# Performance work log

Hardware: AMD Instinct MI355X
Metric: run time of the kernel (lower is better)

The kernel has to match this reference:

```python
import jax, jax.numpy as jnp
import numpy as np

NOT_EPSILON = 1.0

def swishmax(x, axis):
    # x * exp(x - max) normalized by sum(|.|) + 1 over `axis`
    xexp = x * jnp.exp(x - jnp.max(x, axis=axis, keepdims=True))
    return xexp / (jnp.sum(jnp.abs(xexp), axis=axis, keepdims=True) + NOT_EPSILON)

def setup_inputs() -> dict:
    key = jax.random.key(0)
    ks = jax.random.split(key, 8)
    B, S, D = 2, 512, 256
    std = 0.02
    x = jax.random.normal(ks[0], (B, S, D), dtype=jnp.float32)
    w_pre = jax.random.normal(ks[1], (D, D), dtype=jnp.float32) * std
    w_q   = jax.random.normal(ks[2], (D, D), dtype=jnp.float32) * std
    w_k   = jax.random.normal(ks[3], (D, D), dtype=jnp.float32) * std
    w_va  = jax.random.normal(ks[4], (D, D), dtype=jnp.float32) * std
    w_al  = jax.random.normal(ks[5], (D, D), dtype=jnp.float32) * std
    w_vo  = jax.random.normal(ks[6], (D, D), dtype=jnp.float32) * std
    w_end = jax.random.normal(ks[7], (D, D), dtype=jnp.float32) * std
    return {"x": x, "w_pre": w_pre, "w_q": w_q, "w_k": w_k,
            "w_va": w_va, "w_al": w_al, "w_vo": w_vo, "w_end": w_end}

def reference(x, w_pre, w_q, w_k, w_va, w_al, w_vo, w_end):
    # pre: module_1d = Linear(D, D, bias=False)
    X = x @ w_pre.T                                    # [B,S,D]
    # FractalAttention depth=2 (base case): row_dims=(-3,)
    q = X + X @ w_q.T                                  # residual query proj
    k = X + X @ w_k.T                                  # residual key proj
    # batchify: key lhs -> [B,Sk,1,D], query rhs -> [B,1,Sq,D]
    raw = k[:, :, None, :] * q[:, None, :, :]          # [B,Sk,Sq,D]
    logits = raw + raw @ w_al.T                        # residual logit proj over D
    scale = swishmax(logits, axis=-3)                  # normalize over Sk
    v = X + X @ w_va.T
    vs = v[:, :, None, :] * scale                      # [B,Sk,Sq,D]
    vsum = jnp.sum(vs, axis=-3)                        # [B,Sq,D]
    vout = vsum + vsum @ w_vo.T
    X = X + vout                                       # transformer residual
    X = X @ w_end.T                                    # end: module_1d
    return X
```

## Files before the change

### kernel.cpp

```cpp
#include <hip/hip_runtime.h>
#include <hip/hip_bf16.h>


typedef __attribute__((ext_vector_type(8))) short short8;
typedef __attribute__((ext_vector_type(4))) float f32x4;
typedef __attribute__((ext_vector_type(8))) _Float16 half8;
typedef __attribute__((ext_vector_type(4))) _Float16 half4;

#define DD 256
#define SS 512
#define LOG2E 1.4426950408889634f
#define LN2   0.6931471805599453f

__device__ __forceinline__ unsigned short f2bf(float f) {
  unsigned int b = __float_as_uint(f);
  b += 0x7FFFu + ((b >> 16) & 1u);
  return (unsigned short)(b >> 16);
}
__device__ __forceinline__ short8 cvt8(f32x4 lo, f32x4 hi) {
  short8 r;
  r[0]=(short)f2bf(lo[0]); r[1]=(short)f2bf(lo[1]);
  r[2]=(short)f2bf(lo[2]); r[3]=(short)f2bf(lo[3]);
  r[4]=(short)f2bf(hi[0]); r[5]=(short)f2bf(hi[1]);
  r[6]=(short)f2bf(hi[2]); r[7]=(short)f2bf(hi[3]);
  return r;
}
__device__ __forceinline__ void gload16(const void* g, void* l) {
  __builtin_amdgcn_global_load_lds(
      (const __attribute__((address_space(1))) void*)g,
      (__attribute__((address_space(3))) void*)l,
      16, 0, 0);
}

__global__ __launch_bounds__(256) void prep_weights(
    const float* __restrict__ w0, const float* __restrict__ w1,
    const float* __restrict__ w2, const float* __restrict__ w3,
    const float* __restrict__ w4, const float* __restrict__ w5,
    const float* __restrict__ wal, unsigned short* __restrict__ out)
{
  const int bi = blockIdx.x;
  const int m = bi >> 5;
  const int off = ((bi & 31) * 256 + threadIdx.x) * 8;
  const float* src = m==0?w0: m==1?w1: m==2?w2: m==3?w3: m==4?w4: m==5?w5: wal;
  f32x4 a = *(const f32x4*)(src + off);
  f32x4 b = *(const f32x4*)(src + off + 4);
  if (m == 6) {
    const int e = off >> 8, d = off & 255;
#pragma unroll
    for (int jj = 0; jj < 4; ++jj) {
      if (e == d + jj)     a[jj] += 1.0f;
      if (e == d + 4 + jj) b[jj] += 1.0f;
    }
    half8 h;
#pragma unroll
    for (int jj = 0; jj < 4; ++jj) {
      h[jj]     = (_Float16)a[jj];
      h[jj + 4] = (_Float16)b[jj];
    }
    *(half8*)(out + (size_t)m * 65536 + off) = h;
  } else {
    *(short8*)(out + (size_t)m * 65536 + off) = cvt8(a, b);
  }
}

__global__ __launch_bounds__(256) void linear_bf(
    const float* __restrict__ A, const unsigned short* __restrict__ Wbf,
    const float* __restrict__ res1, const float* __restrict__ res2,
    float* __restrict__ out)
{
  const int bi = blockIdx.x;
  const int rb = (bi >> 2) * 16;
  const int cb = (bi & 3) * 64;
  const int tid = threadIdx.x;
  const int wv = tid >> 6, lane = tid & 63;
  const int g = lane >> 4, c = lane & 15;
  const int arow = rb + c;
  const int wrow = cb + wv * 16 + c;

  f32x4 acc = (f32x4){0.f, 0.f, 0.f, 0.f};
#pragma unroll
  for (int ks = 0; ks < 8; ++ks) {
    const int d0 = ks * 32 + g * 8;
    f32x4 a0 = *(const f32x4*)(A + arow * DD + d0);
    f32x4 a1 = *(const f32x4*)(A + arow * DD + d0 + 4);
    short8 av = cvt8(a0, a1);
    short8 bv = *(const short8*)(Wbf + wrow * DD + d0);
    acc = __builtin_amdgcn_mfma_f32_16x16x32_bf16(av, bv, acc, 0, 0, 0);
  }
#pragma unroll
  for (int j = 0; j < 4; ++j) {
    const int ro = rb + g * 4 + j;
    const int co = cb + wv * 16 + c;
    float v = acc[j];
    if (res1) v += res1[ro * DD + co];
    if (res2) v += res2[ro * DD + co];
    out[ro * DD + co] = v;
  }
}

__global__ __launch_bounds__(256) void linear_qkv(
    const float* __restrict__ X,
    const unsigned short* __restrict__ Wq, const unsigned short* __restrict__ Wk,
    const unsigned short* __restrict__ Wv,
    _Float16* __restrict__ qout, _Float16* __restrict__ kout,
    _Float16* __restrict__ vout)
{
  const int bi = blockIdx.x;
  const int rb = (bi >> 2) * 16;
  const int cb = (bi & 3) * 64;
  const int tid = threadIdx.x;
  const int wv = tid >> 6, lane = tid & 63;
  const int g = lane >> 4, c = lane & 15;
  const int arow = rb + c;
  const int wrow = cb + wv * 16 + c;

  f32x4 aq = (f32x4){0.f,0.f,0.f,0.f};
  f32x4 ak = (f32x4){0.f,0.f,0.f,0.f};
  f32x4 av_ = (f32x4){0.f,0.f,0.f,0.f};
#pragma unroll
  for (int ks = 0; ks < 8; ++ks) {
    const int d0 = ks * 32 + g * 8;
    f32x4 a0 = *(const f32x4*)(X + arow * DD + d0);
    f32x4 a1 = *(const f32x4*)(X + arow * DD + d0 + 4);
    short8 af = cvt8(a0, a1);
    short8 bq = *(const short8*)(Wq + wrow * DD + d0);
    aq = __builtin_amdgcn_mfma_f32_16x16x32_bf16(af, bq, aq, 0, 0, 0);
    short8 bk = *(const short8*)(Wk + wrow * DD + d0);
    ak = __builtin_amdgcn_mfma_f32_16x16x32_bf16(af, bk, ak, 0, 0, 0);
    short8 bv = *(const short8*)(Wv + wrow * DD + d0);
    av_ = __builtin_amdgcn_mfma_f32_16x16x32_bf16(af, bv, av_, 0, 0, 0);
  }
#pragma unroll
  for (int j = 0; j < 4; ++j) {
    const int ro = rb + g * 4 + j;
    const int co = cb + wv * 16 + c;
    const float base = X[ro * DD + co];
    qout[ro * DD + co] = (_Float16)((base + aq[j]) * LOG2E);
    kout[ro * DD + co] = (_Float16)(base + ak[j]);
    vout[ro * DD + co] = (_Float16)(base + av_[j]);
  }
}

__global__ __launch_bounds__(256) void pack_kv(
    const _Float16* __restrict__ k, const _Float16* __restrict__ v,
    _Float16* __restrict__ kfrag, _Float16* __restrict__ vfrag)
{
  const int id = blockIdx.x * 256 + threadIdx.x;
  if (id < 32768) {
    const int lane = id & 63, ks = (id >> 6) & 7, t2 = (id >> 9) & 31, b = id >> 14;
    const int g = lane >> 4, c = lane & 15;
    const _Float16* src = k + ((size_t)(b * SS + t2 * 16 + c) * DD + ks * 32 + g * 8);
    *(half8*)(kfrag + (size_t)id * 8) = *(const half8*)src;
  } else {
    const int id2 = id - 32768;
    const int lane = id2 & 63, i = (id2 >> 6) & 1, slice = (id2 >> 7) & 7,
              t2 = (id2 >> 10) & 31, b = id2 >> 15;
    const int g = lane >> 4, c = lane & 15;
    const _Float16* src = v + ((size_t)(b * SS + t2 * 16 + c) * DD + slice * 32 + i * 16 + g * 4);
    *(half4*)(vfrag + (size_t)id2 * 4) = *(const half4*)src;
  }
}

__global__ __launch_bounds__(256, 3) void fractal_attn(
    const _Float16* __restrict__ walI,
    const _Float16* __restrict__ qf,
    const _Float16* __restrict__ kfrag,
    const _Float16* __restrict__ vfrag,
    float* __restrict__ vsum)
{
  __shared__ _Float16 kt[2][4096];

  const int bid = blockIdx.x;
  const int eh = bid & 1;
  const int sq = (bid >> 1) & 511;
  const int b  = bid >> 10;
  const int tid = threadIdx.x;
  const int wv = tid >> 6;
  const int lane = tid & 63;
  const int g = lane >> 4, c = lane & 15;
  const int slice = eh * 4 + wv;
  const int sbase = slice * 32;

  const _Float16* ktile0 = kfrag + (size_t)b * 131072;
  auto stage = [&](int t) {
    const _Float16* src = ktile0 + (size_t)t * 4096;
    _Float16* dst = &kt[t & 1][0];
    gload16(src + tid * 8,        dst + tid * 8);
    gload16(src + 2048 + tid * 8, dst + 2048 + tid * 8);
  };

  stage(0);

  half8 afrag[2][8];
  {
    const _Float16* qrow = qf + (size_t)(b * SS + sq) * DD;
    half8 q8[8];
#pragma unroll
    for (int ks = 0; ks < 8; ++ks)
      q8[ks] = *(const half8*)(qrow + ks * 32 + g * 8);
#pragma unroll
    for (int i = 0; i < 2; ++i) {
      const int e = sbase + i * 16 + c;
      const _Float16* wrow = walI + (size_t)e * DD;
#pragma unroll
      for (int ks = 0; ks < 8; ++ks)
        afrag[i][ks] = (*(const half8*)(wrow + ks * 32 + g * 8)) * q8[ks];
    }
  }

  const _Float16* vfb = vfrag + (size_t)b * 131072 + slice * 512 + lane * 4;

  float mst[8], sst[8], vst[8];
#pragma unroll
  for (int s = 0; s < 8; ++s) { mst[s] = -1e30f; sst[s] = 0.f; vst[s] = 0.f; }

  half8 bf[8];
  half4 vqA[2], vqB[2];
  f32x4 accA[2], accB[2];
  const f32x4 zeroc = (f32x4){0.f, 0.f, 0.f, 0.f};

#define DSREAD(BUF)                                                 \
  {                                                                 \
    const _Float16* kb_ = &kt[BUF][0];                              \
    _Pragma("unroll")                                               \
    for (int ks = 0; ks < 8; ++ks)                                  \
      bf[ks] = *(const half8*)(kb_ + ks * 512 + lane * 8);          \
  }
#define LOADV(T2, VQ)                                               \
  {                                                                 \
    const _Float16* vf_ = vfb + (size_t)(T2) * 4096;                \
    VQ[0] = *(const half4*)(vf_);                                   \
    VQ[1] = *(const half4*)(vf_ + 256);                             \
  }
#define MFMA_INTO(ACC)                                              \
  {                                                                 \
    __builtin_amdgcn_s_setprio(1);                                  \
    ACC[0] = __builtin_amdgcn_mfma_f32_16x16x32_f16(                \
        afrag[0][0], bf[0], zeroc, 0, 0, 0);                        \
    ACC[1] = __builtin_amdgcn_mfma_f32_16x16x32_f16(                \
        afrag[1][0], bf[0], zeroc, 0, 0, 0);                        \
    _Pragma("unroll")                                               \
    for (int ks = 1; ks < 8; ++ks) {                                \
      ACC[0] = __builtin_amdgcn_mfma_f32_16x16x32_f16(              \
          afrag[0][ks], bf[ks], ACC[0], 0, 0, 0);                   \
      ACC[1] = __builtin_amdgcn_mfma_f32_16x16x32_f16(              \
          afrag[1][ks], bf[ks], ACC[1], 0, 0, 0);                   \
    }                                                               \
    __builtin_amdgcn_s_setprio(0);                                  \
  }
#define UPDATE(ACC, VQ)                                             \
  {                                                                 \
    _Pragma("unroll")                                               \
    for (int i = 0; i < 2; ++i)                                     \
      _Pragma("unroll")                                             \
      for (int j = 0; j < 4; ++j) {                                 \
        const int s = i * 4 + j;                                    \
        const float L = ACC[i][j];                                  \
        mst[s] = fmaxf(mst[s], L);                                  \
        const float p = L * __builtin_amdgcn_exp2f(L);              \
        sst[s] += fabsf(p);                                         \
        vst[s] = fmaf((float)VQ[i][j], p, vst[s]);                  \
      }                                                             \
  }

  LOADV(0, vqA);
  __syncthreads();
  DSREAD(0);
  stage(1);
  MFMA_INTO(accA);

#pragma unroll 1
  for (int t = 1; t < 31; t += 2) {
    __syncthreads();
    DSREAD(t & 1);
    LOADV(t, vqB);
    stage(t + 1);
    MFMA_INTO(accB);
    UPDATE(accA, vqA);

    __syncthreads();
    DSREAD((t + 1) & 1);
    LOADV(t + 1, vqA);
    if (t + 2 < 32) stage(t + 2);
    MFMA_INTO(accA);
    UPDATE(accB, vqB);
  }

  __syncthreads();
  DSREAD(1);
  LOADV(31, vqB);
  MFMA_INTO(accB);
  UPDATE(accA, vqA);
  UPDATE(accB, vqB);

#undef DSREAD
#undef LOADV
#undef MFMA_INTO
#undef UPDATE

#pragma unroll
  for (int mask = 1; mask <= 8; mask <<= 1) {
#pragma unroll
    for (int s = 0; s < 8; ++s) {
      mst[s] = fmaxf(mst[s], __shfl_xor(mst[s], mask));
      sst[s] += __shfl_xor(sst[s], mask);
      vst[s] += __shfl_xor(vst[s], mask);
    }
  }

  if (c == 0) {
    float* orow = vsum + (size_t)(b * SS + sq) * DD;
#pragma unroll
    for (int i = 0; i < 2; ++i) {
      f32x4 o;
#pragma unroll
      for (int j = 0; j < 4; ++j) {
        const int s = i * 4 + j;
        const float tt = LN2 * __builtin_amdgcn_exp2f(-mst[s]);
        o[j] = vst[s] * tt / (sst[s] * tt + 1.0f);
      }
      *(f32x4*)(orow + sbase + i * 16 + g * 4) = o;
    }
  }
}

extern "C" void kernel_launch(void* const* d_in, const int* in_sizes, int n_in,
                              void* d_out, int out_size, void* d_ws, size_t ws_size,
                              hipStream_t stream) {
  const float* x     = (const float*)d_in[0];
  const float* w_pre = (const float*)d_in[1];
  const float* w_q   = (const float*)d_in[2];
  const float* w_k   = (const float*)d_in[3];
  const float* w_va  = (const float*)d_in[4];
  const float* w_al  = (const float*)d_in[5];
  const float* w_vo  = (const float*)d_in[6];
  const float* w_end = (const float*)d_in[7];
  float* out = (float*)d_out;

  char* ws = (char*)d_ws;
  float*    X     = (float*)(ws);
  float*    Y     = (float*)(ws + (1 << 20));
  float*    vsum  = (float*)(ws + (2 << 20));
  _Float16* qf16  = (_Float16*)(ws + (3 << 20));
  _Float16* kf16  = (_Float16*)(ws + (3 << 20) + (512 << 10));
  _Float16* vf16  = (_Float16*)(ws + (4 << 20));
  _Float16* kfrag = (_Float16*)(ws + (4 << 20) + (512 << 10));
  _Float16* vfrag = (_Float16*)(ws + (5 << 20));
  unsigned short* wbf = (unsigned short*)(ws + (5 << 20) + (512 << 10));

  prep_weights<<<224, 256, 0, stream>>>(w_pre, w_q, w_k, w_va, w_vo, w_end,
                                        w_al, wbf);
  linear_bf<<<256, 256, 0, stream>>>(x, wbf + 0 * 65536, nullptr, nullptr, X);
  linear_qkv<<<256, 256, 0, stream>>>(X, wbf + 1 * 65536, wbf + 2 * 65536,
                                      wbf + 3 * 65536, qf16, kf16, vf16);
  pack_kv<<<384, 256, 0, stream>>>(kf16, vf16, kfrag, vfrag);
  fractal_attn<<<2048, 256, 0, stream>>>((const _Float16*)(wbf + 6 * 65536),
                                         qf16, kfrag, vfrag, vsum);
  linear_bf<<<256, 256, 0, stream>>>(vsum, wbf + 4 * 65536, vsum, X, Y);
  linear_bf<<<256, 256, 0, stream>>>(Y, wbf + 5 * 65536, nullptr, nullptr, out);
}
```

Before: 120.5 us.

## Stage V tiles through LDS with a four-deep async prefetch pipeline

Deepens the K-tile LDS ring from two to four buffers and adds a matching LDS ring for V fragments. V was previously read directly from global memory per wave; it is now loaded asynchronously alongside K, three tiles ahead. Plain __syncthreads is replaced by explicit vmcnt waits plus s_barrier so loads can stay in flight across iterations. This aims to hide global-memory latency behind the MFMA and exp work. In exchange it uses more LDS per block, which may limit occupancy, and the hand-counted waitcnt values must stay consistent with the number of loads issued.

```diff
diff --git a/kernel.cpp b/kernel.cpp
--- a/kernel.cpp
+++ b/kernel.cpp
@@ -168,7 +168,8 @@
     const _Float16* __restrict__ vfrag,
     float* __restrict__ vsum)
 {
-  __shared__ _Float16 kt[2][4096];
+  __shared__ _Float16 kt[4][4096];
+  __shared__ _Float16 vt[4][2048];
 
   const int bid = blockIdx.x;
   const int eh = bid & 1;
@@ -182,14 +183,18 @@
   const int sbase = slice * 32;
 
   const _Float16* ktile0 = kfrag + (size_t)b * 131072;
+  const _Float16* vtile0 = vfrag + (size_t)b * 131072 + eh * 2048;
   auto stage = [&](int t) {
-    const _Float16* src = ktile0 + (size_t)t * 4096;
-    _Float16* dst = &kt[t & 1][0];
-    gload16(src + tid * 8,        dst + tid * 8);
-    gload16(src + 2048 + tid * 8, dst + 2048 + tid * 8);
+    const _Float16* ks = ktile0 + (size_t)t * 4096;
+    const _Float16* vs = vtile0 + (size_t)t * 4096;
+    _Float16* kd = &kt[t & 3][0];
+    _Float16* vd = &vt[t & 3][0];
+    gload16(ks + tid * 8,        kd + tid * 8);
+    gload16(ks + 2048 + tid * 8, kd + 2048 + tid * 8);
+    gload16(vs + tid * 8,        vd + tid * 8);
   };
 
-  stage(0);
+  stage(0); stage(1); stage(2);
 
   half8 afrag[2][8];
   {
@@ -208,8 +213,6 @@
     }
   }
 
-  const _Float16* vfb = vfrag + (size_t)b * 131072 + slice * 512 + lane * 4;
-
   float mst[8], sst[8], vst[8];
 #pragma unroll
   for (int s = 0; s < 8; ++s) { mst[s] = -1e30f; sst[s] = 0.f; vst[s] = 0.f; }
@@ -219,18 +222,18 @@
   f32x4 accA[2], accB[2];
   const f32x4 zeroc = (f32x4){0.f, 0.f, 0.f, 0.f};
 
-#define DSREAD(BUF)                                                 \
+#define DSREAD(T)                                                   \
   {                                                                 \
-    const _Float16* kb_ = &kt[BUF][0];                              \
+    const _Float16* kb_ = &kt[(T) & 3][0];                          \
     _Pragma("unroll")                                               \
     for (int ks = 0; ks < 8; ++ks)                                  \
       bf[ks] = *(const half8*)(kb_ + ks * 512 + lane * 8);          \
   }
-#define LOADV(T2, VQ)                                               \
+#define DSVREAD(T, VQ)                                              \
   {                                                                 \
-    const _Float16* vf_ = vfb + (size_t)(T2) * 4096;                \
-    VQ[0] = *(const half4*)(vf_);                                   \
-    VQ[1] = *(const half4*)(vf_ + 256);                             \
+    const _Float16* vb_ = &vt[(T) & 3][0];                          \
+    VQ[0] = *(const half4*)(vb_ + wv * 512 + lane * 4);             \
+    VQ[1] = *(const half4*)(vb_ + wv * 512 + 256 + lane * 4);       \
   }
 #define MFMA_INTO(ACC)                                              \
   {                                                                 \
@@ -262,41 +265,49 @@
         vst[s] = fmaf((float)VQ[i][j], p, vst[s]);                  \
       }                                                             \
   }
-
-  LOADV(0, vqA);
-  __syncthreads();
-  DSREAD(0);
-  stage(1);
+#define WAIT(N) asm volatile("s_waitcnt vmcnt(" #N ")" ::: "memory")
+
+  WAIT(6); __builtin_amdgcn_s_barrier();
+  stage(3);
+  DSREAD(0); DSVREAD(0, vqA);
   MFMA_INTO(accA);
 
 #pragma unroll 1
-  for (int t = 1; t < 31; t += 2) {
-    __syncthreads();
-    DSREAD(t & 1);
-    LOADV(t, vqB);
-    stage(t + 1);
+  for (int t = 1; t < 29; t += 2) {
+    WAIT(6); __builtin_amdgcn_s_barrier();
+    stage(t + 3);
+    DSREAD(t); DSVREAD(t, vqB);
     MFMA_INTO(accB);
     UPDATE(accA, vqA);
 
-    __syncthreads();
-    DSREAD((t + 1) & 1);
-    LOADV(t + 1, vqA);
-    if (t + 2 < 32) stage(t + 2);
+    WAIT(6); __builtin_amdgcn_s_barrier();
+    if (t + 4 < 32) stage(t + 4);
+    DSREAD(t + 1); DSVREAD(t + 1, vqA);
     MFMA_INTO(accA);
     UPDATE(accB, vqB);
   }
 
-  __syncthreads();
-  DSREAD(1);
-  LOADV(31, vqB);
+  WAIT(6); __builtin_amdgcn_s_barrier();
+  DSREAD(29); DSVREAD(29, vqB);
+  MFMA_INTO(accB);
+  UPDATE(accA, vqA);
+
+  WAIT(3); __builtin_amdgcn_s_barrier();
+  DSREAD(30); DSVREAD(30, vqA);
+  MFMA_INTO(accA);
+  UPDATE(accB, vqB);
+
+  WAIT(0); __builtin_amdgcn_s_barrier();
+  DSREAD(31); DSVREAD(31, vqB);
   MFMA_INTO(accB);
   UPDATE(accA, vqA);
   UPDATE(accB, vqB);
 
 #undef DSREAD
-#undef LOADV
+#undef DSVREAD
 #undef MFMA_INTO
 #undef UPDATE
+#undef WAIT
 
 #pragma unroll
   for (int mask = 1; mask <= 8; mask <<= 1) {
```

New measurement: 126.5 us. 1.05x slower.
